# Kernel tuning notes

Hardware: AMD Instinct MI355X
Metric: run time of the kernel (lower is better)

The kernel has to match this reference:

```python
import jax, jax.numpy as jnp
import numpy as np

D_IN, D_HIDDEN, D_OUT, BATCH = 128, 512, 128, 65536


def setup_inputs() -> dict:
    key = jax.random.key(0)
    k_x, k_u, k_a, k_b, k_c = jax.random.split(key, 5)
    return {
        "x": jax.random.normal(k_x, (BATCH, D_HIDDEN), dtype=jnp.float32),
        "u": jax.random.normal(k_u, (BATCH, D_IN), dtype=jnp.float32),
        "a": jax.random.normal(k_a, (D_HIDDEN,), dtype=jnp.float32),
        "b": jax.random.normal(k_b, (D_IN, D_HIDDEN), dtype=jnp.float32),
        "c": jax.random.normal(k_c, (D_HIDDEN, D_OUT), dtype=jnp.float32),
    }


def reference(x, u, a, b, c):
    # Diagonal linear RNN step: new state = decay * x + u @ b, then output GEMM.
    decay = jax.nn.softmax(a)  # [d_hidden]
    x_new = x * decay[None, :] + u @ b  # [B, d_hidden]
    output = x_new @ c  # [B, d_out]
    return (x_new, output)
```

## Files before the change

kernel.cpp:

```cpp
#include <hip/hip_runtime.h>
#include <hip/hip_bf16.h>

#define BATCH 65536
#define DIN   128
#define DH    512
#define DOUT  128
#define ROWS  32

typedef __attribute__((ext_vector_type(4))) float f32x4;
typedef __attribute__((ext_vector_type(8))) short s16x8;

__device__ __forceinline__ ushort f32_to_bf16_rn(float f) {
    uint32_t u = __float_as_uint(f);
    uint32_t r = (u + 0x7FFFu + ((u >> 16) & 1u)) >> 16;
    return (ushort)r;
}
__device__ __forceinline__ float bf16_to_f32(ushort h) {
    return __uint_as_float(((uint32_t)h) << 16);
}
__device__ __forceinline__ f32x4 mfma16(s16x8 a, s16x8 b, f32x4 c) {
    return __builtin_amdgcn_mfma_f32_16x16x32_bf16(a, b, c, 0, 0, 0);
}
__device__ __forceinline__ s16x8 cvt8(f32x4 v0, f32x4 v1) {
    s16x8 r;
#pragma unroll
    for (int j = 0; j < 4; ++j) r[j] = (short)f32_to_bf16_rn(v0[j]);
#pragma unroll
    for (int j = 0; j < 4; ++j) r[4 + j] = (short)f32_to_bf16_rn(v1[j]);
    return r;
}

__global__ void prep_kernel(const float* __restrict__ a,
                            const float* __restrict__ b,
                            const float* __restrict__ c,
                            float* __restrict__ decay,
                            ushort* __restrict__ bhi,
                            ushort* __restrict__ chi)
{
    const int t = threadIdx.x;
    if (blockIdx.x == 0) {
        __shared__ float red[256];
        float v0 = a[t], v1 = a[t + 256];
        red[t] = fmaxf(v0, v1);
        __syncthreads();
        for (int s = 128; s > 0; s >>= 1) {
            if (t < s) red[t] = fmaxf(red[t], red[t + s]);
            __syncthreads();
        }
        float M = red[0];
        __syncthreads();
        float e0 = expf(v0 - M), e1 = expf(v1 - M);
        red[t] = e0 + e1;
        __syncthreads();
        for (int s = 128; s > 0; s >>= 1) {
            if (t < s) red[t] += red[t + s];
            __syncthreads();
        }
        float S = red[0];
        decay[t]       = e0 / S;
        decay[t + 256] = e1 / S;
    } else {
        const int p = (blockIdx.x - 1) * 256 + t;
        const int mtx = p >> 13;
        const int q = p & 8191;
        const int f = q >> 6;
        const int l = q & 63;
        s16x8 hi;
        if (mtx == 0) {
            const int cg = f >> 2, ks = f & 3;
            const int col = cg * 16 + (l & 15);
            const int kbase = ks * 32 + (l >> 4) * 8;
#pragma unroll
            for (int j = 0; j < 8; ++j)
                hi[j] = (short)f32_to_bf16_rn(b[(size_t)(kbase + j) * DH + col]);
            *(s16x8*)(bhi + (size_t)q * 8) = hi;
        } else {
            const int cg = f >> 4, ks = f & 15;
            const int col = cg * 16 + (l & 15);
            const int kbase = ks * 32 + (l >> 4) * 8;
#pragma unroll
            for (int j = 0; j < 8; ++j)
                hi[j] = (short)f32_to_bf16_rn(c[(size_t)(kbase + j) * DOUT + col]);
            *(s16x8*)(chi + (size_t)q * 8) = hi;
        }
    }
}

__global__ __launch_bounds__(256, 4)
void rnn_fused(const float* __restrict__ u, const float* __restrict__ x,
               const float* __restrict__ decay,
               const ushort* __restrict__ bhi, const ushort* __restrict__ chi,
               float* __restrict__ xn, float* __restrict__ out)
{
    __shared__ __align__(16) char smem[16384];
    ushort* Ah = (ushort*)smem;

    const int t = threadIdx.x;
    const int lane = t & 63, wc = t >> 6;
    const int cl = lane & 15, hk = lane >> 4;
    const int row0 = blockIdx.x * ROWS;

    {
        const int r = t >> 3;
        const int kb = (t & 7) * 2;
#pragma unroll
        for (int i = 0; i < 2; ++i) {
            const float* src = u + (size_t)(row0 + r) * DIN + (kb + i) * 8;
            f32x4 v0 = *(const f32x4*)src;
            f32x4 v1 = *(const f32x4*)(src + 4);
            const int byte = (r * 256 + (kb + i) * 16) ^ ((r & 7) << 4);
            *(s16x8*)((char*)Ah + byte) = cvt8(v0, v1);
        }
    }

    s16x8 bF[4], bFn[4];
#pragma unroll
    for (int ks = 0; ks < 4; ++ks)
        bF[ks] = *(const s16x8*)(bhi + (size_t)(wc * 4 + ks) * 512 + lane * 8);

    float xv[2][4], xvn[2][4], dvc, dvn;
    dvc = decay[wc * 16 + cl];
#pragma unroll
    for (int mf = 0; mf < 2; ++mf)
#pragma unroll
        for (int j = 0; j < 4; ++j)
            xv[mf][j] = x[(size_t)(row0 + mf * 16 + 4 * hk + j) * DH + wc * 16 + cl];

    __syncthreads();

    f32x4 acc2[2][2];
#pragma unroll
    for (int mf = 0; mf < 2; ++mf)
#pragma unroll
        for (int nf = 0; nf < 2; ++nf)
            acc2[mf][nf] = (f32x4){0.f, 0.f, 0.f, 0.f};

    for (int ct = 0; ct < 8; ++ct) {
        char* Xh = smem + 8192 + (ct & 1) * 4096;

        s16x8 cF[2][2];
#pragma unroll
        for (int ks2 = 0; ks2 < 2; ++ks2)
#pragma unroll
            for (int nf = 0; nf < 2; ++nf)
                cF[ks2][nf] = *(const s16x8*)(chi +
                    (size_t)((wc * 2 + nf) * 16 + ct * 2 + ks2) * 512 + lane * 8);

        f32x4 acc1[2];
        acc1[0] = (f32x4){0.f, 0.f, 0.f, 0.f};
        acc1[1] = (f32x4){0.f, 0.f, 0.f, 0.f};
#pragma unroll
        for (int ks = 0; ks < 4; ++ks) {
            const int ko = ks * 32 + hk * 8;
            s16x8 ah[2];
#pragma unroll
            for (int mf = 0; mf < 2; ++mf) {
                const int r = mf * 16 + cl;
                const int byte = (r * 256 + ko * 2) ^ ((r & 7) << 4);
                ah[mf] = *(const s16x8*)((const char*)Ah + byte);
            }
#pragma unroll
            for (int mf = 0; mf < 2; ++mf) acc1[mf] = mfma16(ah[mf], bF[ks], acc1[mf]);
        }

        if (ct < 7) {
#pragma unroll
            for (int ks = 0; ks < 4; ++ks)
                bFn[ks] = *(const s16x8*)(bhi +
                    (size_t)(((ct + 1) * 4 + wc) * 4 + ks) * 512 + lane * 8);
            const int ncol = (ct + 1) * 64 + wc * 16 + cl;
            dvn = decay[ncol];
#pragma unroll
            for (int mf = 0; mf < 2; ++mf)
#pragma unroll
                for (int j = 0; j < 4; ++j)
                    xvn[mf][j] = x[(size_t)(row0 + mf * 16 + 4 * hk + j) * DH + ncol];
        }

        {
            const int col = ct * 64 + wc * 16 + cl;
#pragma unroll
            for (int mf = 0; mf < 2; ++mf) {
#pragma unroll
                for (int j = 0; j < 4; ++j) {
                    const int rl = mf * 16 + 4 * hk + j;
                    const float v = acc1[mf][j] + dvc * xv[mf][j];
                    xn[(size_t)(row0 + rl) * DH + col] = v;
                    const int cbyte = (rl * 128 + (wc * 16 + cl) * 2) ^ ((rl & 7) << 4);
                    *(ushort*)(Xh + cbyte) = f32_to_bf16_rn(v);
                }
            }
        }

        __syncthreads();

#pragma unroll
        for (int ks2 = 0; ks2 < 2; ++ks2) {
            const int ko = ks2 * 32 + hk * 8;
            s16x8 ah2[2];
#pragma unroll
            for (int mf = 0; mf < 2; ++mf) {
                const int r = mf * 16 + cl;
                const int byte = (r * 128 + ko * 2) ^ ((r & 7) << 4);
                ah2[mf] = *(const s16x8*)((const char*)Xh + byte);
            }
#pragma unroll
            for (int nf = 0; nf < 2; ++nf)
#pragma unroll
                for (int mf = 0; mf < 2; ++mf)
                    acc2[mf][nf] = mfma16(ah2[mf], cF[ks2][nf], acc2[mf][nf]);
        }

#pragma unroll
        for (int ks = 0; ks < 4; ++ks) bF[ks] = bFn[ks];
        dvc = dvn;
#pragma unroll
        for (int mf = 0; mf < 2; ++mf)
#pragma unroll
            for (int j = 0; j < 4; ++j) xv[mf][j] = xvn[mf][j];
    }

#pragma unroll
    for (int nf = 0; nf < 2; ++nf) {
        const int ocol = wc * 32 + nf * 16 + cl;
#pragma unroll
        for (int mf = 0; mf < 2; ++mf) {
#pragma unroll
            for (int j = 0; j < 4; ++j) {
                const int rl = mf * 16 + 4 * hk + j;
                out[(size_t)(row0 + rl) * DOUT + ocol] = acc2[mf][nf][j];
            }
        }
    }
}

extern "C" void kernel_launch(void* const* d_in, const int* in_sizes, int n_in,
                              void* d_out, int out_size, void* d_ws, size_t ws_size,
                              hipStream_t stream)
{
    const float* x = (const float*)d_in[0];
    const float* u = (const float*)d_in[1];
    const float* a = (const float*)d_in[2];
    const float* b = (const float*)d_in[3];
    const float* c = (const float*)d_in[4];

    float* xn  = (float*)d_out;
    float* out = xn + (size_t)BATCH * DH;

    char* ws = (char*)d_ws;
    float*  decay = (float*)ws;
    ushort* bhi = (ushort*)(ws + 4096);
    ushort* chi = bhi + 128 * 512;

    prep_kernel<<<dim3(65), dim3(256), 0, stream>>>(a, b, c, decay, bhi, chi);
    rnn_fused<<<dim3(BATCH / ROWS), dim3(256), 0, stream>>>(u, x, decay, bhi, chi, xn, out);
}
```

Baseline: 103.3 us.

## Split output GEMM via precomputed B·C so blocks compute x_new and output independently

Precomputes B@C (128x128) in a prep kernel and rewrites output as (decay*x)@C + u@(B@C). Each batch tile is then handled by two independent blocks, one producing x_new and one producing the output, which removes the serial dependency and per-tile barriers between the two GEMMs. The cost is that x and u are read twice, shared memory grows to 40KB, and the output block does a K=512 GEMM plus a K=128 GEMM. An extra prep launch is also added.

```diff
diff --git a/kernel.cpp b/kernel.cpp
--- a/kernel.cpp
+++ b/kernel.cpp
@@ -30,12 +30,13 @@
     return r;
 }
 
-__global__ void prep_kernel(const float* __restrict__ a,
-                            const float* __restrict__ b,
-                            const float* __restrict__ c,
-                            float* __restrict__ decay,
-                            ushort* __restrict__ bhi,
-                            ushort* __restrict__ chi)
+__global__ void prep1_kernel(const float* __restrict__ a,
+                             const float* __restrict__ b,
+                             const float* __restrict__ c,
+                             float* __restrict__ decay,
+                             ushort* __restrict__ bhi,
+                             ushort* __restrict__ chi,
+                             float* __restrict__ bcf)
 {
     const int t = threadIdx.x;
     if (blockIdx.x == 0) {
@@ -59,7 +60,7 @@
         float S = red[0];
         decay[t]       = e0 / S;
         decay[t + 256] = e1 / S;
-    } else {
+    } else if (blockIdx.x <= 64) {
         const int p = (blockIdx.x - 1) * 256 + t;
         const int mtx = p >> 13;
         const int q = p & 8191;
@@ -83,72 +84,185 @@
                 hi[j] = (short)f32_to_bf16_rn(c[(size_t)(kbase + j) * DOUT + col]);
             *(s16x8*)(chi + (size_t)q * 8) = hi;
         }
+    } else {
+        const int i = (blockIdx.x - 65) * 2 + (t >> 7);
+        const int j = t & 127;
+        float acc = 0.f;
+        for (int k = 0; k < DH; ++k)
+            acc = fmaf(b[(size_t)i * DH + k], c[(size_t)k * DOUT + j], acc);
+        bcf[i * DOUT + j] = acc;
     }
+}
+
+__global__ void prep2_kernel(const float* __restrict__ bcf,
+                             ushort* __restrict__ bch)
+{
+    const int p = blockIdx.x * 256 + threadIdx.x;
+    const int f = p >> 6, l = p & 63;
+    const int cg = f >> 2, ks = f & 3;
+    const int col = cg * 16 + (l & 15);
+    const int kbase = ks * 32 + (l >> 4) * 8;
+    s16x8 hi;
+#pragma unroll
+    for (int j = 0; j < 8; ++j)
+        hi[j] = (short)f32_to_bf16_rn(bcf[(size_t)(kbase + j) * DOUT + col]);
+    *(s16x8*)(bch + (size_t)p * 8) = hi;
 }
 
 __global__ __launch_bounds__(256, 4)
 void rnn_fused(const float* __restrict__ u, const float* __restrict__ x,
                const float* __restrict__ decay,
                const ushort* __restrict__ bhi, const ushort* __restrict__ chi,
+               const ushort* __restrict__ bch,
                float* __restrict__ xn, float* __restrict__ out)
 {
-    __shared__ __align__(16) char smem[16384];
-    ushort* Ah = (ushort*)smem;
+    __shared__ __align__(16) char smem[40960];
 
     const int t = threadIdx.x;
     const int lane = t & 63, wc = t >> 6;
     const int cl = lane & 15, hk = lane >> 4;
-    const int row0 = blockIdx.x * ROWS;
-
-    {
-        const int r = t >> 3;
-        const int kb = (t & 7) * 2;
-#pragma unroll
-        for (int i = 0; i < 2; ++i) {
-            const float* src = u + (size_t)(row0 + r) * DIN + (kb + i) * 8;
-            f32x4 v0 = *(const f32x4*)src;
-            f32x4 v1 = *(const f32x4*)(src + 4);
-            const int byte = (r * 256 + (kb + i) * 16) ^ ((r & 7) << 4);
-            *(s16x8*)((char*)Ah + byte) = cvt8(v0, v1);
-        }
-    }
-
-    s16x8 bF[4], bFn[4];
-#pragma unroll
-    for (int ks = 0; ks < 4; ++ks)
-        bF[ks] = *(const s16x8*)(bhi + (size_t)(wc * 4 + ks) * 512 + lane * 8);
-
-    float xv[2][4], xvn[2][4], dvc, dvn;
-    dvc = decay[wc * 16 + cl];
-#pragma unroll
-    for (int mf = 0; mf < 2; ++mf)
-#pragma unroll
-        for (int j = 0; j < 4; ++j)
-            xv[mf][j] = x[(size_t)(row0 + mf * 16 + 4 * hk + j) * DH + wc * 16 + cl];
-
-    __syncthreads();
-
-    f32x4 acc2[2][2];
-#pragma unroll
-    for (int mf = 0; mf < 2; ++mf)
-#pragma unroll
-        for (int nf = 0; nf < 2; ++nf)
-            acc2[mf][nf] = (f32x4){0.f, 0.f, 0.f, 0.f};
-
-    for (int ct = 0; ct < 8; ++ct) {
-        char* Xh = smem + 8192 + (ct & 1) * 4096;
-
-        s16x8 cF[2][2];
-#pragma unroll
-        for (int ks2 = 0; ks2 < 2; ++ks2)
+    const int rb = blockIdx.x >> 1;
+    const int row0 = rb * ROWS;
+
+    if ((blockIdx.x & 1) == 0) {
+        ushort* Ah = (ushort*)smem;
+        {
+            const int r = t >> 3;
+            const int kb = (t & 7) * 2;
+#pragma unroll
+            for (int i = 0; i < 2; ++i) {
+                const float* src = u + (size_t)(row0 + r) * DIN + (kb + i) * 8;
+                f32x4 v0 = *(const f32x4*)src;
+                f32x4 v1 = *(const f32x4*)(src + 4);
+                const int byte = (r * 256 + (kb + i) * 16) ^ ((r & 7) << 4);
+                *(s16x8*)((char*)Ah + byte) = cvt8(v0, v1);
+            }
+        }
+
+        s16x8 bF[4], bFn[4];
+#pragma unroll
+        for (int ks = 0; ks < 4; ++ks)
+            bF[ks] = *(const s16x8*)(bhi + (size_t)(wc * 4 + ks) * 512 + lane * 8);
+        float xv[2][4], xvn[2][4], dvc, dvn;
+        dvc = decay[wc * 16 + cl];
+#pragma unroll
+        for (int mf = 0; mf < 2; ++mf)
+#pragma unroll
+            for (int j = 0; j < 4; ++j)
+                xv[mf][j] = x[(size_t)(row0 + mf * 16 + 4 * hk + j) * DH + wc * 16 + cl];
+
+        __syncthreads();
+
+        for (int ct = 0; ct < 8; ++ct) {
+            if (ct < 7) {
+#pragma unroll
+                for (int ks = 0; ks < 4; ++ks)
+                    bFn[ks] = *(const s16x8*)(bhi +
+                        (size_t)(((ct + 1) * 4 + wc) * 4 + ks) * 512 + lane * 8);
+                const int ncol = (ct + 1) * 64 + wc * 16 + cl;
+                dvn = decay[ncol];
+#pragma unroll
+                for (int mf = 0; mf < 2; ++mf)
+#pragma unroll
+                    for (int j = 0; j < 4; ++j)
+                        xvn[mf][j] = x[(size_t)(row0 + mf * 16 + 4 * hk + j) * DH + ncol];
+            }
+
+            f32x4 acc1[2];
+            acc1[0] = (f32x4){0.f, 0.f, 0.f, 0.f};
+            acc1[1] = (f32x4){0.f, 0.f, 0.f, 0.f};
+#pragma unroll
+            for (int ks = 0; ks < 4; ++ks) {
+                const int ko = ks * 32 + hk * 8;
+                s16x8 ah[2];
+#pragma unroll
+                for (int mf = 0; mf < 2; ++mf) {
+                    const int r = mf * 16 + cl;
+                    const int byte = (r * 256 + ko * 2) ^ ((r & 7) << 4);
+                    ah[mf] = *(const s16x8*)((const char*)Ah + byte);
+                }
+#pragma unroll
+                for (int mf = 0; mf < 2; ++mf) acc1[mf] = mfma16(ah[mf], bF[ks], acc1[mf]);
+            }
+
+            {
+                const int col = ct * 64 + wc * 16 + cl;
+#pragma unroll
+                for (int mf = 0; mf < 2; ++mf)
+#pragma unroll
+                    for (int j = 0; j < 4; ++j)
+                        xn[(size_t)(row0 + mf * 16 + 4 * hk + j) * DH + col] =
+                            acc1[mf][j] + dvc * xv[mf][j];
+            }
+
+#pragma unroll
+            for (int ks = 0; ks < 4; ++ks) bF[ks] = bFn[ks];
+            dvc = dvn;
+#pragma unroll
+            for (int mf = 0; mf < 2; ++mf)
+#pragma unroll
+                for (int j = 0; j < 4; ++j) xv[mf][j] = xvn[mf][j];
+        }
+    } else {
+        ushort* Au = (ushort*)smem;
+        char*   Xs = smem + 8192;
+
+        {
+            const int r = t >> 3;
+            const int kb = (t & 7) * 2;
+#pragma unroll
+            for (int i = 0; i < 2; ++i) {
+                const float* src = u + (size_t)(row0 + r) * DIN + (kb + i) * 8;
+                f32x4 v0 = *(const f32x4*)src;
+                f32x4 v1 = *(const f32x4*)(src + 4);
+                const int byte = (r * 256 + (kb + i) * 16) ^ ((r & 7) << 4);
+                *(s16x8*)((char*)Au + byte) = cvt8(v0, v1);
+            }
+        }
+        {
+            const int r2 = t >> 3;
+            const int c0 = (t & 7) * 8;
+            const float* xrow = x + (size_t)(row0 + r2) * DH + c0;
+#pragma unroll
+            for (int ct = 0; ct < 8; ++ct) {
+                const int col = ct * 64 + c0;
+                f32x4 v0 = *(const f32x4*)(xrow + ct * 64);
+                f32x4 v1 = *(const f32x4*)(xrow + ct * 64 + 4);
+                const f32x4 d0 = *(const f32x4*)&decay[col];
+                const f32x4 d1 = *(const f32x4*)&decay[col + 4];
+                const int byte = (r2 * 1024 + col * 2) ^ ((r2 & 7) << 4);
+                *(s16x8*)(Xs + byte) = cvt8(v0 * d0, v1 * d1);
+            }
+        }
+        __syncthreads();
+
+        f32x4 acc[2][2];
+#pragma unroll
+        for (int mf = 0; mf < 2; ++mf)
 #pragma unroll
             for (int nf = 0; nf < 2; ++nf)
-                cF[ks2][nf] = *(const s16x8*)(chi +
-                    (size_t)((wc * 2 + nf) * 16 + ct * 2 + ks2) * 512 + lane * 8);
-
-        f32x4 acc1[2];
-        acc1[0] = (f32x4){0.f, 0.f, 0.f, 0.f};
-        acc1[1] = (f32x4){0.f, 0.f, 0.f, 0.f};
+                acc[mf][nf] = (f32x4){0.f, 0.f, 0.f, 0.f};
+
+#pragma unroll
+        for (int ksg = 0; ksg < 16; ++ksg) {
+            const int ko = ksg * 32 + hk * 8;
+            s16x8 ah[2];
+#pragma unroll
+            for (int mf = 0; mf < 2; ++mf) {
+                const int r = mf * 16 + cl;
+                const int byte = (r * 1024 + ko * 2) ^ ((r & 7) << 4);
+                ah[mf] = *(const s16x8*)(Xs + byte);
+            }
+#pragma unroll
+            for (int nf = 0; nf < 2; ++nf) {
+                const s16x8 cF = *(const s16x8*)(chi +
+                    (size_t)((wc * 2 + nf) * 16 + ksg) * 512 + lane * 8);
+#pragma unroll
+                for (int mf = 0; mf < 2; ++mf)
+                    acc[mf][nf] = mfma16(ah[mf], cF, acc[mf][nf]);
+            }
+        }
+
 #pragma unroll
         for (int ks = 0; ks < 4; ++ks) {
             const int ko = ks * 32 + hk * 8;
@@ -157,79 +271,27 @@
             for (int mf = 0; mf < 2; ++mf) {
                 const int r = mf * 16 + cl;
                 const int byte = (r * 256 + ko * 2) ^ ((r & 7) << 4);
-                ah[mf] = *(const s16x8*)((const char*)Ah + byte);
-            }
-#pragma unroll
-            for (int mf = 0; mf < 2; ++mf) acc1[mf] = mfma16(ah[mf], bF[ks], acc1[mf]);
-        }
-
-        if (ct < 7) {
-#pragma unroll
-            for (int ks = 0; ks < 4; ++ks)
-                bFn[ks] = *(const s16x8*)(bhi +
-                    (size_t)(((ct + 1) * 4 + wc) * 4 + ks) * 512 + lane * 8);
-            const int ncol = (ct + 1) * 64 + wc * 16 + cl;
-            dvn = decay[ncol];
+                ah[mf] = *(const s16x8*)((const char*)Au + byte);
+            }
+#pragma unroll
+            for (int nf = 0; nf < 2; ++nf) {
+                const s16x8 bcF = *(const s16x8*)(bch +
+                    (size_t)((wc * 2 + nf) * 4 + ks) * 512 + lane * 8);
+#pragma unroll
+                for (int mf = 0; mf < 2; ++mf)
+                    acc[mf][nf] = mfma16(ah[mf], bcF, acc[mf][nf]);
+            }
+        }
+
+#pragma unroll
+        for (int nf = 0; nf < 2; ++nf) {
+            const int ocol = wc * 32 + nf * 16 + cl;
 #pragma unroll
             for (int mf = 0; mf < 2; ++mf)
 #pragma unroll
                 for (int j = 0; j < 4; ++j)
-                    xvn[mf][j] = x[(size_t)(row0 + mf * 16 + 4 * hk + j) * DH + ncol];
-        }
-
-        {
-            const int col = ct * 64 + wc * 16 + cl;
-#pragma unroll
-            for (int mf = 0; mf < 2; ++mf) {
-#pragma unroll
-                for (int j = 0; j < 4; ++j) {
-                    const int rl = mf * 16 + 4 * hk + j;
-                    const float v = acc1[mf][j] + dvc * xv[mf][j];
-                    xn[(size_t)(row0 + rl) * DH + col] = v;
-                    const int cbyte = (rl * 128 + (wc * 16 + cl) * 2) ^ ((rl & 7) << 4);
-                    *(ushort*)(Xh + cbyte) = f32_to_bf16_rn(v);
-                }
-            }
-        }
-
-        __syncthreads();
-
-#pragma unroll
-        for (int ks2 = 0; ks2 < 2; ++ks2) {
-            const int ko = ks2 * 32 + hk * 8;
-            s16x8 ah2[2];
-#pragma unroll
-            for (int mf = 0; mf < 2; ++mf) {
-                const int r = mf * 16 + cl;
-                const int byte = (r * 128 + ko * 2) ^ ((r & 7) << 4);
-                ah2[mf] = *(const s16x8*)((const char*)Xh + byte);
-            }
-#pragma unroll
-            for (int nf = 0; nf < 2; ++nf)
-#pragma unroll
-                for (int mf = 0; mf < 2; ++mf)
-                    acc2[mf][nf] = mfma16(ah2[mf], cF[ks2][nf], acc2[mf][nf]);
-        }
-
-#pragma unroll
-        for (int ks = 0; ks < 4; ++ks) bF[ks] = bFn[ks];
-        dvc = dvn;
-#pragma unroll
-        for (int mf = 0; mf < 2; ++mf)
-#pragma unroll
-            for (int j = 0; j < 4; ++j) xv[mf][j] = xvn[mf][j];
-    }
-
-#pragma unroll
-    for (int nf = 0; nf < 2; ++nf) {
-        const int ocol = wc * 32 + nf * 16 + cl;
-#pragma unroll
-        for (int mf = 0; mf < 2; ++mf) {
-#pragma unroll
-            for (int j = 0; j < 4; ++j) {
-                const int rl = mf * 16 + 4 * hk + j;
-                out[(size_t)(row0 + rl) * DOUT + ocol] = acc2[mf][nf][j];
-            }
+                    out[(size_t)(row0 + mf * 16 + 4 * hk + j) * DOUT + ocol] =
+                        acc[mf][nf][j];
         }
     }
 }
@@ -251,7 +313,10 @@
     float*  decay = (float*)ws;
     ushort* bhi = (ushort*)(ws + 4096);
     ushort* chi = bhi + 128 * 512;
-
-    prep_kernel<<<dim3(65), dim3(256), 0, stream>>>(a, b, c, decay, bhi, chi);
-    rnn_fused<<<dim3(BATCH / ROWS), dim3(256), 0, stream>>>(u, x, decay, bhi, chi, xn, out);
-}
+    float*  bcf = (float*)(ws + 4096 + 2 * 131072);
+    ushort* bch = (ushort*)(ws + 4096 + 2 * 131072 + 65536);
+
+    prep1_kernel<<<dim3(129), dim3(256), 0, stream>>>(a, b, c, decay, bhi, chi, bcf);
+    prep2_kernel<<<dim3(8), dim3(256), 0, stream>>>(bcf, bch);
+    rnn_fused<<<dim3(BATCH / ROWS * 2), dim3(256), 0, stream>>>(u, x, decay, bhi, chi, bch, xn, out);
+}
```

Result: slower. 136.7 us (+32.3%).
